# Optimization experiments

Hardware: AMD Instinct MI355X
Metric: run time of the kernel (lower is better)

The kernel has to match this reference:

```python
import jax, jax.numpy as jnp
import numpy as np

B = 256
D_MODEL = 2048
D_STATE = 128
D_CONV = 4
EXPAND = 2
HEADDIM = 64
D_INNER = EXPAND * D_MODEL          # 4096
NHEADS = D_INNER // HEADDIM         # 64
CONV_DIM = D_INNER + 2 * D_STATE    # 4352
D_IN_PROJ = 2 * D_INNER + 2 * D_STATE + NHEADS  # 8512
EPS = 1e-5


def setup_inputs() -> dict:
    key = jax.random.key(0)
    ks = jax.random.split(key, 10)
    rn = lambda k, shp, s=1.0: jax.random.normal(k, shp, jnp.float32) * s
    # dt_bias initialized like the torch module: inverse-softplus of dt ~ U[log 1e-3, log 1e-1]
    u = jax.random.uniform(ks[5], (NHEADS,), jnp.float32)
    dt = jnp.exp(u * (np.log(0.1) - np.log(0.001)) + np.log(0.001))
    dt = jnp.clip(dt, 1e-4, None)
    dt_bias = dt + jnp.log(-jnp.expm1(-dt))
    A_log = jnp.log(jax.random.uniform(ks[6], (NHEADS,), jnp.float32, minval=1.0, maxval=1.1))
    return {
        "hidden_states": rn(ks[0], (B, 1, D_MODEL)),
        "conv_state": rn(ks[1], (B, CONV_DIM, D_CONV)),
        "ssm_state": rn(ks[2], (B, NHEADS, HEADDIM, D_STATE), 0.1),
        "W_in": rn(ks[3], (D_IN_PROJ, D_MODEL), 0.02),
        "conv_w": rn(ks[4], (CONV_DIM, D_CONV), 0.1),  # conv1d.weight 'd 1 w' squeezed
        "conv_b": jnp.zeros((CONV_DIM,), jnp.float32),
        "dt_bias": dt_bias,
        "A_log": A_log,
        "D": jnp.ones((NHEADS,), jnp.float32),
        "norm_w": jnp.ones((D_INNER,), jnp.float32),
        "W_out": rn(ks[7], (D_MODEL, D_INNER), 0.02),
    }


def reference(hidden_states, conv_state, ssm_state, W_in, conv_w, conv_b,
              dt_bias, A_log, D, norm_w, W_out):
    h = hidden_states[:, 0, :]                    # [B, d_model]
    zxbcdt = h @ W_in.T                           # [B, d_in_proj]; d_mlp = 0
    z = zxbcdt[:, :D_INNER]
    xBC = zxbcdt[:, D_INNER:D_INNER + CONV_DIM]
    dt = zxbcdt[:, D_INNER + CONV_DIM:]           # [B, nheads]

    # roll conv buffer, append new token, depthwise conv over window
    cs = jnp.concatenate([conv_state[:, :, 1:], xBC[:, :, None]], axis=-1)  # [B, conv_dim, d_conv]
    xBC = jnp.sum(cs * conv_w[None, :, :], axis=-1) + conv_b
    xBC = jax.nn.silu(xBC)

    x = xBC[:, :D_INNER]
    Bm = xBC[:, D_INNER:D_INNER + D_STATE]        # [B, d_state]
    C = xBC[:, D_INNER + D_STATE:]                # [B, d_state]

    A = -jnp.exp(A_log)                           # [nheads]
    dt = jax.nn.softplus(dt + dt_bias)            # [B, nheads]
    dA = jnp.exp(dt * A)                          # [B, nheads]

    xh = x.reshape(B, NHEADS, HEADDIM)            # [B, h, p]
    dBx = jnp.einsum('bh,bn,bhp->bhpn', dt, Bm, xh)
    ss = ssm_state * dA[:, :, None, None] + dBx   # [B, h, p, n]
    y = jnp.einsum('bhpn,bn->bhp', ss, C) + D[None, :, None] * xh
    y = y.reshape(B, D_INNER)

    # gated RMSNorm (gate before norm, single group)
    y = y * jax.nn.silu(z)
    y = y * jax.lax.rsqrt(jnp.mean(y * y, axis=-1, keepdims=True) + EPS) * norm_w

    out = y @ W_out.T                             # [B, d_model]
    return out[:, None, :]
```

## Files before the change

kernel.cpp:

```cpp
#include <hip/hip_runtime.h>
#include <hip/hip_bf16.h>
#include <math.h>

#define BATCH     256
#define DMODEL    2048
#define DSTATE    128
#define HEADDIM_  64
#define DINNER    4096
#define NHEADS_   64
#define CONVDIM   4352
#define DINPROJ   8512
#define EPS_      1e-5f

typedef __attribute__((ext_vector_type(8))) short short8;
typedef __attribute__((ext_vector_type(4))) short short4v;
typedef __attribute__((ext_vector_type(4))) float f32x4;

__device__ __forceinline__ short bfbits(float f) {
    __hip_bfloat16 h = __float2bfloat16(f);
    return *reinterpret_cast<short*>(&h);
}
__device__ __forceinline__ short8 cvt8(float4 a, float4 b) {
    short8 r;
    r[0] = bfbits(a.x); r[1] = bfbits(a.y); r[2] = bfbits(a.z); r[3] = bfbits(a.w);
    r[4] = bfbits(b.x); r[5] = bfbits(b.y); r[6] = bfbits(b.z); r[7] = bfbits(b.w);
    return r;
}
__device__ __forceinline__ int swz(int row, int cb) {
    return row * 128 + (cb ^ ((row & 7) << 4));
}

__global__ __launch_bounds__(256)
void f2b(const float* __restrict__ in, short* __restrict__ o) {
    int i = (blockIdx.x * 256 + threadIdx.x) * 8;
    float4 a = *(const float4*)(in + i);
    float4 b = *(const float4*)(in + i + 4);
    *(short8*)(o + i) = cvt8(a, b);
}

template<int TH, int BN>
__global__ __launch_bounds__(TH, 2)
void gemm_mfma(const short* __restrict__ A, const float* __restrict__ W,
               float* __restrict__ C, int lda, int ldb, int ldc, int kc) {
    constexpr int WNC = BN / 32;
    constexpr int ASL = 2048 / TH;
    constexpr int BBYTES = BN * 128;
    const int bn0 = blockIdx.x * BN;
    const int k0  = blockIdx.z * kc;
    C += (size_t)blockIdx.z * 256 * ldc;
    const int t = threadIdx.x;
    const int lane = t & 63;
    const int w = t >> 6;
    const int wm = w / WNC, wn = w % WNC;
    const int fr = lane & 15, fg = lane >> 4;

    __shared__ __align__(16) char lds[2][32768 + BBYTES];

    const short* apb[ASL]; int ao[ASL];
    #pragma unroll
    for (int i = 0; i < ASL; ++i) {
        int s = t + TH * i, r = s >> 3, sl = s & 7;
        apb[i] = A + (size_t)r * lda + k0 + sl * 8;
        ao[i] = swz(r, sl * 16);
    }
    const int br = t >> 3, bsl = t & 7;
    const float* bp = W + (size_t)(bn0 + br) * ldb + k0 + bsl * 8;
    const int bo = 32768 + swz(br, bsl * 16);

    int aro[4], bro[2];
    #pragma unroll
    for (int m = 0; m < 4; ++m) aro[m] = swz(wm * 64 + m * 16 + fr, fg * 16);
    #pragma unroll
    for (int n = 0; n < 2; ++n) bro[n] = 32768 + swz(wn * 32 + n * 16 + fr, fg * 16);

    f32x4 acc[4][2] = {};
    short8 rab[ASL];
    float4 rb0, rb1;

    #define LOADT(kt) { const int ko = (kt) << 6;                                \
        _Pragma("unroll") for (int i = 0; i < ASL; ++i)                          \
            rab[i] = *(const short8*)(apb[i] + ko);                              \
        rb0 = *(const float4*)(bp + ko); rb1 = *(const float4*)(bp + ko + 4); }
    #define STAGET(buf) {                                                        \
        _Pragma("unroll") for (int i = 0; i < ASL; ++i)                          \
            *(short8*)(lds[buf] + ao[i]) = rab[i];                               \
        *(short8*)(lds[buf] + bo) = cvt8(rb0, rb1); }

    LOADT(0);
    STAGET(0);
    int cur = 0;
    const int nT = kc >> 6;
    for (int kt = 0; kt < nT; ++kt) {
        if (kt + 1 < nT) LOADT(kt + 1);
        __syncthreads();
        #pragma unroll
        for (int ks = 0; ks < 2; ++ks) {
            short8 af[4], bf[2];
            #pragma unroll
            for (int m = 0; m < 4; ++m) af[m] = *(short8*)(lds[cur] + (aro[m] ^ (ks << 6)));
            #pragma unroll
            for (int n = 0; n < 2; ++n) bf[n] = *(short8*)(lds[cur] + (bro[n] ^ (ks << 6)));
            #pragma unroll
            for (int m = 0; m < 4; ++m)
                #pragma unroll
                for (int n = 0; n < 2; ++n)
                    acc[m][n] = __builtin_amdgcn_mfma_f32_16x16x32_bf16(af[m], bf[n], acc[m][n], 0, 0, 0);
        }
        if (kt + 1 < nT) STAGET(cur ^ 1);
        cur ^= 1;
    }
    #pragma unroll
    for (int m = 0; m < 4; ++m)
        #pragma unroll
        for (int n = 0; n < 2; ++n) {
            const int row = wm * 64 + m * 16 + fg * 4;
            const int col = bn0 + wn * 32 + n * 16 + fr;
            #pragma unroll
            for (int j = 0; j < 4; ++j)
                C[(size_t)(row + j) * ldc + col] = acc[m][n][j];
        }
    #undef LOADT
    #undef STAGET
}

__global__ __launch_bounds__(256)
void reduce4(const float* __restrict__ part, float* __restrict__ out) {
    const int i = (blockIdx.x * 256 + threadIdx.x) * 4;
    float4 s = *(const float4*)(part + i);
    #pragma unroll
    for (int k = 1; k < 4; ++k) {
        float4 p = *(const float4*)(part + (size_t)k * BATCH * DMODEL + i);
        s.x += p.x; s.y += p.y; s.z += p.z; s.w += p.w;
    }
    *(float4*)(out + i) = s;
}

__global__ __launch_bounds__(1024)
void fused_mid(const float* __restrict__ zp0, const float* __restrict__ zp1,
               const float* __restrict__ conv_state,
               const float* __restrict__ conv_w, const float* __restrict__ conv_b,
               const float* __restrict__ dt_bias, const float* __restrict__ A_log,
               const float* __restrict__ ssm, const float* __restrict__ Dp,
               const float* __restrict__ nw, short* __restrict__ yn) {
    const int b = blockIdx.x, t = threadIdx.x;
    const int lane = t & 63, w = t >> 6;
    __shared__ float sxbc[CONVDIM];
    __shared__ float sy[DINNER];
    __shared__ float sred[16];
    __shared__ float sdA[NHEADS_], scoef[NHEADS_];

    #pragma unroll
    for (int it = 0; it < 5; ++it) {
        int c = it * 1024 + t;
        if (c < CONVDIM) {
            float4 cs = *(const float4*)&conv_state[((size_t)b * CONVDIM + c) * 4];
            float4 w4 = *(const float4*)&conv_w[c * 4];
            float xin = zp0[(size_t)b * DINPROJ + DINNER + c]
                      + zp1[(size_t)b * DINPROJ + DINNER + c];
            float v = cs.y * w4.x + cs.z * w4.y + cs.w * w4.z + xin * w4.w + conv_b[c];
            sxbc[c] = v / (1.f + expf(-v));
        }
    }
    __syncthreads();

    if (t < 128) {
        float prod = sxbc[DINNER + t] * sxbc[DINNER + DSTATE + t];
        #pragma unroll
        for (int m = 1; m < 64; m <<= 1) prod += __shfl_xor(prod, m);
        if ((t & 63) == 0) sred[t >> 6] = prod;
    }
    __syncthreads();
    if (t < NHEADS_) {
        float BC = sred[0] + sred[1];
        float x = zp0[(size_t)b * DINPROJ + DINNER + CONVDIM + t]
                + zp1[(size_t)b * DINPROJ + DINNER + CONVDIM + t] + dt_bias[t];
        float dt = (x > 20.f) ? x : log1pf(expf(x));
        sdA[t] = expf(dt * (-expf(A_log[t])));
        scoef[t] = dt * BC + Dp[t];
    }
    __syncthreads();

    {
        const int pq = lane >> 4, nl = lane & 15;
        const float4 c4a = *(const float4*)&sxbc[DINNER + DSTATE + nl * 8];
        const float4 c4b = *(const float4*)&sxbc[DINNER + DSTATE + nl * 8 + 4];
        #pragma unroll
        for (int k = 0; k < 4; ++k) {
            const int h = w * 4 + k;
            const float* S = ssm + (((size_t)b * NHEADS_ + h) * HEADDIM_) * DSTATE;
            const float dA = sdA[h], coef = scoef[h];
            #pragma unroll 8
            for (int pp = 0; pp < 16; ++pp) {
                const int p = pp * 4 + pq;
                f32x4 sa = __builtin_nontemporal_load((const f32x4*)&S[p * DSTATE + nl * 8]);
                f32x4 sb = __builtin_nontemporal_load((const f32x4*)&S[p * DSTATE + nl * 8 + 4]);
                float dot = sa[0] * c4a.x + sa[1] * c4a.y + sa[2] * c4a.z + sa[3] * c4a.w
                          + sb[0] * c4b.x + sb[1] * c4b.y + sb[2] * c4b.z + sb[3] * c4b.w;
                #pragma unroll
                for (int m = 1; m < 16; m <<= 1) dot += __shfl_xor(dot, m);
                if (nl == 0)
                    sy[h * HEADDIM_ + p] = dA * dot + sxbc[h * HEADDIM_ + p] * coef;
            }
        }
    }
    __syncthreads();

    {
        const int i = t * 4;
        float4 yv = *(const float4*)&sy[i];
        float4 z0 = *(const float4*)&zp0[(size_t)b * DINPROJ + i];
        float4 z1 = *(const float4*)&zp1[(size_t)b * DINPROJ + i];
        float4 zv = { z0.x + z1.x, z0.y + z1.y, z0.z + z1.z, z0.w + z1.w };
        float4 g;
        g.x = yv.x * (zv.x / (1.f + expf(-zv.x)));
        g.y = yv.y * (zv.y / (1.f + expf(-zv.y)));
        g.z = yv.z * (zv.z / (1.f + expf(-zv.z)));
        g.w = yv.w * (zv.w / (1.f + expf(-zv.w)));
        float ss = g.x * g.x + g.y * g.y + g.z * g.z + g.w * g.w;
        #pragma unroll
        for (int m = 1; m < 64; m <<= 1) ss += __shfl_xor(ss, m);
        __syncthreads();
        if (lane == 0) sred[w] = ss;
        __syncthreads();
        float tot = 0.f;
        #pragma unroll
        for (int k = 0; k < 16; ++k) tot += sred[k];
        const float sc = rsqrtf(tot * (1.f / DINNER) + EPS_);
        float4 w4 = *(const float4*)&nw[i];
        short4v o;
        o[0] = bfbits(g.x * sc * w4.x); o[1] = bfbits(g.y * sc * w4.y);
        o[2] = bfbits(g.z * sc * w4.z); o[3] = bfbits(g.w * sc * w4.w);
        *(short4v*)&yn[(size_t)b * DINNER + i] = o;
    }
}

extern "C" void kernel_launch(void* const* d_in, const int* in_sizes, int n_in,
                              void* d_out, int out_size, void* d_ws, size_t ws_size,
                              hipStream_t stream) {
    const float* hid        = (const float*)d_in[0];
    const float* conv_state = (const float*)d_in[1];
    const float* ssm        = (const float*)d_in[2];
    const float* W_in       = (const float*)d_in[3];
    const float* conv_w     = (const float*)d_in[4];
    const float* conv_b     = (const float*)d_in[5];
    const float* dt_bias    = (const float*)d_in[6];
    const float* A_log      = (const float*)d_in[7];
    const float* Dp         = (const float*)d_in[8];
    const float* norm_w     = (const float*)d_in[9];
    const float* W_out      = (const float*)d_in[10];
    float* out = (float*)d_out;

    float* ws    = (float*)d_ws;
    float* zpart = ws;
    float* part  = zpart + (size_t)2 * BATCH * DINPROJ;
    short* hidbf = (short*)(part + (size_t)4 * BATCH * DMODEL);
    short* yn_bf = hidbf + (size_t)BATCH * DMODEL;

    f2b<<<dim3(BATCH * DMODEL / 2048), 256, 0, stream>>>(hid, hidbf);
    gemm_mfma<512, 64><<<dim3(DINPROJ / 64, 1, 2), 512, 0, stream>>>(
        hidbf, W_in, zpart, DMODEL, DMODEL, DINPROJ, DMODEL / 2);
    fused_mid<<<dim3(BATCH), 1024, 0, stream>>>(
        zpart, zpart + (size_t)BATCH * DINPROJ,
        conv_state, conv_w, conv_b, dt_bias, A_log, ssm, Dp, norm_w, yn_bf);
    gemm_mfma<256, 32><<<dim3(DMODEL / 32, 1, 4), 256, 0, stream>>>(
        yn_bf, W_out, part, DINNER, DINNER, DMODEL, DINNER / 4);
    reduce4<<<dim3(BATCH * DMODEL / 1024), 256, 0, stream>>>(part, out);
}
```

Baseline: 148.4 us.

## Fuse hidden-state bf16 conversion into in-proj GEMM and retile out-proj split-K

Removes the standalone f2b conversion kernel by letting the in-projection GEMM load fp32 activations and convert them to bf16 while staging into LDS. The out-projection GEMM switches from 256-thread/32-column tiles with 4-way split-K to 512-thread/64-column tiles with 8-way split-K, and the reduction kernel now sums 8 partials. This saves one launch and one activation round trip, but doubles the A-load register footprint in the first GEMM and doubles the partial-sum traffic in the reduction.

```diff
diff --git a/kernel.cpp b/kernel.cpp
--- a/kernel.cpp
+++ b/kernel.cpp
@@ -30,17 +30,9 @@
     return row * 128 + (cb ^ ((row & 7) << 4));
 }
 
-__global__ __launch_bounds__(256)
-void f2b(const float* __restrict__ in, short* __restrict__ o) {
-    int i = (blockIdx.x * 256 + threadIdx.x) * 8;
-    float4 a = *(const float4*)(in + i);
-    float4 b = *(const float4*)(in + i + 4);
-    *(short8*)(o + i) = cvt8(a, b);
-}
-
-template<int TH, int BN>
+template<int TH, int BN, bool ACVT>
 __global__ __launch_bounds__(TH, 2)
-void gemm_mfma(const short* __restrict__ A, const float* __restrict__ W,
+void gemm_mfma(const void* __restrict__ Av, const float* __restrict__ W,
                float* __restrict__ C, int lda, int ldb, int ldc, int kc) {
     constexpr int WNC = BN / 32;
     constexpr int ASL = 2048 / TH;
@@ -56,11 +48,12 @@
 
     __shared__ __align__(16) char lds[2][32768 + BBYTES];
 
-    const short* apb[ASL]; int ao[ASL];
+    const short* apb[ASL]; const float* apf[ASL]; int ao[ASL];
     #pragma unroll
     for (int i = 0; i < ASL; ++i) {
         int s = t + TH * i, r = s >> 3, sl = s & 7;
-        apb[i] = A + (size_t)r * lda + k0 + sl * 8;
+        if (ACVT) apf[i] = (const float*)Av + (size_t)r * lda + k0 + sl * 8;
+        else      apb[i] = (const short*)Av + (size_t)r * lda + k0 + sl * 8;
         ao[i] = swz(r, sl * 16);
     }
     const int br = t >> 3, bsl = t & 7;
@@ -75,15 +68,19 @@
 
     f32x4 acc[4][2] = {};
     short8 rab[ASL];
+    float4 raf[ASL][2];
     float4 rb0, rb1;
 
     #define LOADT(kt) { const int ko = (kt) << 6;                                \
-        _Pragma("unroll") for (int i = 0; i < ASL; ++i)                          \
-            rab[i] = *(const short8*)(apb[i] + ko);                              \
+        _Pragma("unroll") for (int i = 0; i < ASL; ++i) {                        \
+            if (ACVT) { raf[i][0] = *(const float4*)(apf[i] + ko);               \
+                        raf[i][1] = *(const float4*)(apf[i] + ko + 4); }         \
+            else rab[i] = *(const short8*)(apb[i] + ko); }                       \
         rb0 = *(const float4*)(bp + ko); rb1 = *(const float4*)(bp + ko + 4); }
     #define STAGET(buf) {                                                        \
         _Pragma("unroll") for (int i = 0; i < ASL; ++i)                          \
-            *(short8*)(lds[buf] + ao[i]) = rab[i];                               \
+            *(short8*)(lds[buf] + ao[i]) = ACVT ? cvt8(raf[i][0], raf[i][1])     \
+                                                : rab[i];                        \
         *(short8*)(lds[buf] + bo) = cvt8(rb0, rb1); }
 
     LOADT(0);
@@ -124,11 +121,11 @@
 }
 
 __global__ __launch_bounds__(256)
-void reduce4(const float* __restrict__ part, float* __restrict__ out) {
+void reduce8(const float* __restrict__ part, float* __restrict__ out) {
     const int i = (blockIdx.x * 256 + threadIdx.x) * 4;
     float4 s = *(const float4*)(part + i);
     #pragma unroll
-    for (int k = 1; k < 4; ++k) {
+    for (int k = 1; k < 8; ++k) {
         float4 p = *(const float4*)(part + (size_t)k * BATCH * DMODEL + i);
         s.x += p.x; s.y += p.y; s.z += p.z; s.w += p.w;
     }
@@ -253,16 +250,14 @@
     float* ws    = (float*)d_ws;
     float* zpart = ws;
     float* part  = zpart + (size_t)2 * BATCH * DINPROJ;
-    short* hidbf = (short*)(part + (size_t)4 * BATCH * DMODEL);
-    short* yn_bf = hidbf + (size_t)BATCH * DMODEL;
-
-    f2b<<<dim3(BATCH * DMODEL / 2048), 256, 0, stream>>>(hid, hidbf);
-    gemm_mfma<512, 64><<<dim3(DINPROJ / 64, 1, 2), 512, 0, stream>>>(
-        hidbf, W_in, zpart, DMODEL, DMODEL, DINPROJ, DMODEL / 2);
+    short* yn_bf = (short*)(part + (size_t)8 * BATCH * DMODEL);
+
+    gemm_mfma<512, 64, true><<<dim3(DINPROJ / 64, 1, 2), 512, 0, stream>>>(
+        hid, W_in, zpart, DMODEL, DMODEL, DINPROJ, DMODEL / 2);
     fused_mid<<<dim3(BATCH), 1024, 0, stream>>>(
         zpart, zpart + (size_t)BATCH * DINPROJ,
         conv_state, conv_w, conv_b, dt_bias, A_log, ssm, Dp, norm_w, yn_bf);
-    gemm_mfma<256, 32><<<dim3(DMODEL / 32, 1, 4), 256, 0, stream>>>(
-        yn_bf, W_out, part, DINNER, DINNER, DMODEL, DINNER / 4);
-    reduce4<<<dim3(BATCH * DMODEL / 1024), 256, 0, stream>>>(part, out);
-}
+    gemm_mfma<512, 64, false><<<dim3(DMODEL / 64, 1, 8), 512, 0, stream>>>(
+        yn_bf, W_out, part, DINNER, DINNER, DMODEL, DINNER / 8);
+    reduce8<<<dim3(BATCH * DMODEL / 1024), 256, 0, stream>>>(part, out);
+}
```

New measurement: 151.2 us. About the same (+1.9%).
